# Optimization experiments

Measured on AMD Instinct MI355X. Metric: run time of the kernel, lower is better.

## Reference

```python
import jax, jax.numpy as jnp
import numpy as np
from jax import lax

B, S, D, N_ORDER, K = 8, 4096, 256, 2, 3
G = N_ORDER + 1  # groups in HyenaProjection
EPS_FILT = 1e-8


def setup_inputs() -> dict:
    key = jax.random.key(0)
    ks = jax.random.split(key, 8)
    sc = 0.02
    # positions: per-row arange with trailing -1 padding (one contiguous read per row)
    vl = jnp.where(jnp.arange(B) % 2 == 0, S, (3 * S) // 4)
    pos = jnp.where(jnp.arange(S, dtype=jnp.int32)[None, :] < vl[:, None],
                    jnp.arange(S, dtype=jnp.int32)[None, :], -1)
    return {
        "embeddings": jax.random.normal(ks[0], (B, S, D), jnp.float32),
        "positions": pos,
        "W_proj": jax.random.normal(ks[1], (D, G * D), jnp.float32) * sc,
        "conv_w": jax.random.normal(ks[2], (G * D, D, K), jnp.float32) * sc,
        "conv_b": jnp.zeros((G * D,), jnp.float32),
        "W1": jax.random.normal(ks[3], (D, D), jnp.float32) * sc,
        "b1": jnp.zeros((D,), jnp.float32),
        "ln_g": jnp.ones((D,), jnp.float32),
        "ln_b": jnp.zeros((D,), jnp.float32),
        "W2": jax.random.normal(ks[4], (D, N_ORDER * D), jnp.float32) * sc,
        "b2": jnp.zeros((N_ORDER * D,), jnp.float32),
        "ff_scale": jnp.ones((1, 1, N_ORDER * D), jnp.float32),
        "W_out": jax.random.normal(ks[5], (D, D), jnp.float32) * sc,
        "b_out": jnp.zeros((D,), jnp.float32),
    }


def adjust_positions(pos):
    pf = jnp.where(pos == -1, jnp.inf, pos.astype(jnp.float32))
    minp = pf.min(axis=-1, keepdims=True)
    adj = pos.astype(jnp.float32) - minp
    return jnp.where(pos == -1, -1.0, adj)


def rope_rotate(x, adj_pos):
    # compute_theta_vector + compute_rotation_angles + apply_dimensionwise_rotation
    d2 = x.shape[-1] // 2
    theta = 1.0 / (10000.0 ** (jnp.arange(d2, dtype=jnp.float32) / d2))
    ang = adj_pos[..., None] * theta  # (b, s, d/2)
    cos, sin = jnp.cos(ang), jnp.sin(ang)
    x1, x2 = x[..., 0::2], x[..., 1::2]
    r1 = x1 * cos - x2 * sin
    r2 = x1 * sin + x2 * cos
    return jnp.stack([r1, r2], axis=-1).reshape(x.shape)


def feed_forward(x, W1, b1, ln_g, ln_b, W2, b2, ff_scale):
    h = x @ W1 + b1
    mu = h.mean(-1, keepdims=True)
    var = ((h - mu) ** 2).mean(-1, keepdims=True)
    h = (h - mu) / jnp.sqrt(var + 1e-5) * ln_g + ln_b
    h = jax.nn.gelu(h, approximate=False)
    return (h @ W2 + b2) * ff_scale


def fft_long_conv(x, f, mask):
    # x, f: (b, d, s); 2L zero-padded circular conv == linear conv; torch norm='forward' pair => /n net
    L = x.shape[-1]
    n = 2 * L
    y = jnp.fft.irfft(jnp.fft.rfft(x, n=n) * jnp.fft.rfft(f, n=n), n=n)[..., :L] / n
    return y * mask[:, None, :]


def reference(embeddings, positions, W_proj, conv_w, conv_b, W1, b1, ln_g, ln_b, W2, b2, ff_scale, W_out, b_out):
    mask = (positions != -1).astype(embeddings.dtype)  # (b, s)

    # HyenaProjection: linear -> grouped short conv -> mask -> split into G streams
    z = jnp.einsum('bsd,de->bes', embeddings, W_proj)  # (b, G*d, s)
    z = lax.conv_general_dilated(z, conv_w, (1,), [(K // 2, K // 2)],
                                 dimension_numbers=('NCH', 'OIH', 'NCH'),
                                 feature_group_count=G)
    z = (z + conv_b[None, :, None]) * mask[:, None, :]
    zs = jnp.split(z, G, axis=1)  # G tensors of (b, d, s)

    # HyenaFilter: RoPE -> FFN -> reshape (b, n, d, s) -> L1 normalize over d
    t = rope_rotate(embeddings, adjust_positions(positions))
    h_hat = feed_forward(t, W1, b1, ln_g, ln_b, W2, b2, ff_scale)  # (b, s, n*d)
    h_hat = h_hat.reshape(h_hat.shape[0], h_hat.shape[1], N_ORDER, D).transpose(0, 2, 3, 1)
    h_hat = h_hat / (jnp.sum(jnp.abs(h_hat), axis=2, keepdims=True) + EPS_FILT)

    # Hyena recurrence with FFT long convolutions
    v = zs[-1]
    for i in range(N_ORDER):
        v = zs[i] * fft_long_conv(v, h_hat[:, i], mask)

    out = jnp.einsum('bds,de->bse', v, W_out) + b_out
    return out * mask[..., None]  # reassemble leaves padded positions zero
```

## Files before the change

### kernel.cpp

```cpp
#include <hip/hip_runtime.h>
#include <cstdint>

#define S_LEN 4096
#define D_DIM 256

#define OFF_MINP 0
#define OFF_WPT  16
#define OFF_WTH  (OFF_WPT + 768*256)
#define OFF_WTL  (OFF_WTH + 294912)
#define OFF_C    (OFF_WTL + 294912)
#define OFF_HH   (OFF_C + 8*768*4096)
#define OFF_V    (OFF_HH + 8*2*256*4096)
#define OFF_U    (OFF_V + 8*256*4096)


typedef __attribute__((ext_vector_type(8))) short short8;
typedef __attribute__((ext_vector_type(4))) float f32x4;

__device__ __forceinline__ unsigned int f2bf(float x) {
    union { float f; unsigned int u; } v; v.f = x;
    unsigned int r = v.u + 0x7fffu + ((v.u >> 16) & 1u);
    return r >> 16;
}
__device__ __forceinline__ float bf2f(unsigned int h) {
    union { unsigned int u; float f; } v; v.u = h << 16; return v.f;
}

__global__ __launch_bounds__(256) void k_minpos(const int* __restrict__ pos, float* __restrict__ minp)
{
    const int b = blockIdx.x;
    const int tid = threadIdx.x;
    int mn = 0x7fffffff;
    const int* p = pos + (size_t)b * S_LEN;
    for (int s = tid; s < S_LEN; s += 256) {
        const int v = p[s];
        if (v != -1) mn = min(mn, v);
    }
    __shared__ int red[256];
    red[tid] = mn;
    __syncthreads();
    for (int st = 128; st > 0; st >>= 1) {
        if (tid < st) red[tid] = min(red[tid], red[tid + st]);
        __syncthreads();
    }
    if (tid == 0) minp[b] = (float)red[0];
}

__global__ __launch_bounds__(256) void k_wpt(const float* __restrict__ Wp, float* __restrict__ WpT)
{
    __shared__ float t[32][33];
    const int e0 = blockIdx.x * 32;
    const int d0 = blockIdx.y * 32;
    const int lx = threadIdx.x & 31, ly = threadIdx.x >> 5;
#pragma unroll
    for (int q = 0; q < 4; ++q)
        t[ly + 8*q][lx] = Wp[(size_t)(d0 + ly + 8*q) * 768 + e0 + lx];
    __syncthreads();
#pragma unroll
    for (int q = 0; q < 4; ++q)
        WpT[(size_t)(e0 + ly + 8*q) * 256 + d0 + lx] = t[lx][ly + 8*q];
}

__global__ __launch_bounds__(256) void k_tsplit(const float* __restrict__ W, const int K, const int N,
                                                unsigned short* __restrict__ oh, unsigned short* __restrict__ ol)
{
    __shared__ float t[32][33];
    const int n0 = blockIdx.x * 32;
    const int k0 = blockIdx.y * 32;
    const int lx = threadIdx.x & 31, ly = threadIdx.x >> 5;
#pragma unroll
    for (int q = 0; q < 4; ++q)
        t[ly + 8*q][lx] = W[(size_t)(k0 + ly + 8*q) * N + n0 + lx];
    __syncthreads();
#pragma unroll
    for (int q = 0; q < 4; ++q) {
        const float v = t[lx][ly + 8*q];
        const unsigned int h = f2bf(v);
        oh[(size_t)(n0 + ly + 8*q) * K + k0 + lx] = (unsigned short)h;
        ol[(size_t)(n0 + ly + 8*q) * K + k0 + lx] = (unsigned short)f2bf(v - bf2f(h));
    }
}

__global__ __launch_bounds__(256) void k_weff(const float* __restrict__ WpT, const float* __restrict__ cw,
                                              unsigned short* __restrict__ wth, unsigned short* __restrict__ wtl)
{
    const int o = blockIdx.x;
    const int d = threadIdx.x;
    const int g = o >> 8;
    __shared__ float cwrow[768];
    for (int i = threadIdx.x; i < 768; i += 256) cwrow[i] = cw[(size_t)o * 768 + i];
    __syncthreads();
    float a0 = 0.f, a1 = 0.f, a2 = 0.f;
    const float* wb = WpT + (size_t)(g * 256) * 256 + d;
#pragma unroll 4
    for (int i = 0; i < 256; ++i) {
        const float wv = wb[(size_t)i * 256];
        a0 += wv * cwrow[i*3+0];
        a1 += wv * cwrow[i*3+1];
        a2 += wv * cwrow[i*3+2];
    }
    const float av[3] = {a0, a1, a2};
#pragma unroll
    for (int t = 0; t < 3; ++t) {
        const unsigned int hb = f2bf(av[t]);
        const unsigned int lb = f2bf(av[t] - bf2f(hb));
        wth[(size_t)o * 768 + t * 256 + d] = (unsigned short)hb;
        wtl[(size_t)o * 768 + t * 256 + d] = (unsigned short)lb;
    }
}

#define CG_LDA 40
__global__ __launch_bounds__(256, 3) void k_convgemm(
    const float* __restrict__ emb, const int* __restrict__ pos,
    const unsigned short* __restrict__ wth, const unsigned short* __restrict__ wtl,
    const float* __restrict__ convb, float* __restrict__ c)
{
    const int b  = blockIdx.z;
    const int o0 = blockIdx.y * 128;
    const int s0 = blockIdx.x * 128;
    const int tid  = threadIdx.x;
    const int wave = tid >> 6, lane = tid & 63;
    const int m16  = lane & 15, quad = lane >> 4;

    __shared__ __align__(16) unsigned short As[130 * CG_LDA];
    __shared__ __align__(16) unsigned short Bh[128 * CG_LDA];
    __shared__ __align__(16) unsigned short Bl[128 * CG_LDA];

    const int rA = tid >> 1;
    const int cA = (tid & 1) * 16;
    const int srowA = s0 + rA - 1;
    const bool vA = (srowA >= 0 && srowA < S_LEN);
    const float* embA = emb + ((size_t)b * S_LEN + (vA ? srowA : 0)) * D_DIM + cA;
    const int rT = 128 + (tid >> 3);
    const int cT = (tid & 7) * 4;
    const int srowT = s0 + rT - 1;
    const bool vT = (tid < 16) && (srowT >= 0 && srowT < S_LEN);
    const float* embT = emb + ((size_t)b * S_LEN + ((tid < 16 && vT) ? srowT : 0)) * D_DIM + cT;

    const int rB0 = tid >> 2,        gB0 = (tid & 3) * 8;
    const int rB1 = 64 + (tid >> 2), gB1 = gB0;

    float4 apf[4]; float4 apfT;
    uint4 bph0, bpl0, bph1, bpl1;

#pragma unroll
    for (int q = 0; q < 4; ++q) apf[q] = vA ? *(const float4*)(embA + q * 4) : make_float4(0.f,0.f,0.f,0.f);
    apfT = vT ? *(const float4*)(embT) : make_float4(0.f,0.f,0.f,0.f);
    {
        const size_t gi0 = (size_t)(o0 + rB0) * 768 + gB0;
        const size_t gi1 = (size_t)(o0 + rB1) * 768 + gB1;
        bph0 = *(const uint4*)(wth + gi0); bpl0 = *(const uint4*)(wtl + gi0);
        bph1 = *(const uint4*)(wth + gi1); bpl1 = *(const uint4*)(wtl + gi1);
    }

    f32x4 acc[2][8];
#pragma unroll
    for (int mt = 0; mt < 2; ++mt)
#pragma unroll
        for (int nt = 0; nt < 8; ++nt)
#pragma unroll
            for (int e = 0; e < 4; ++e) acc[mt][nt][e] = 0.f;

    for (int c8 = 0; c8 < 8; ++c8) {
        for (int t = 0; t < 3; ++t) {
            __syncthreads();
            if (t == 0) {
#pragma unroll
                for (int q = 0; q < 4; ++q) {
                    const float4 v = apf[q];
                    uint2 hp;
                    hp.x = f2bf(v.x) | (f2bf(v.y) << 16);
                    hp.y = f2bf(v.z) | (f2bf(v.w) << 16);
                    *(uint2*)&As[rA * CG_LDA + cA + q * 4] = hp;
                }
                if (tid < 16) {
                    const float4 v = apfT;
                    uint2 hp;
                    hp.x = f2bf(v.x) | (f2bf(v.y) << 16);
                    hp.y = f2bf(v.z) | (f2bf(v.w) << 16);
                    *(uint2*)&As[rT * CG_LDA + cT] = hp;
                }
                if (c8 < 7) {
                    const int base = (c8 + 1) * 32;
#pragma unroll
                    for (int q = 0; q < 4; ++q) apf[q] = vA ? *(const float4*)(embA + base + q * 4) : make_float4(0.f,0.f,0.f,0.f);
                    apfT = vT ? *(const float4*)(embT + base) : make_float4(0.f,0.f,0.f,0.f);
                }
            }
            *(uint4*)&Bh[rB0 * CG_LDA + gB0] = bph0;
            *(uint4*)&Bl[rB0 * CG_LDA + gB0] = bpl0;
            *(uint4*)&Bh[rB1 * CG_LDA + gB1] = bph1;
            *(uint4*)&Bl[rB1 * CG_LDA + gB1] = bpl1;
            if (!(c8 == 7 && t == 2)) {
                const int t2  = (t == 2) ? 0 : (t + 1);
                const int c82 = c8 + (t == 2);
                const int kbase = t2 * 256 + c82 * 32;
                const size_t gi0 = (size_t)(o0 + rB0) * 768 + kbase + gB0;
                const size_t gi1 = (size_t)(o0 + rB1) * 768 + kbase + gB1;
                bph0 = *(const uint4*)(wth + gi0); bpl0 = *(const uint4*)(wtl + gi0);
                bph1 = *(const uint4*)(wth + gi1); bpl1 = *(const uint4*)(wtl + gi1);
            }
            __syncthreads();
            short8 ah[2];
#pragma unroll
            for (int mt = 0; mt < 2; ++mt) {
                const int ar = (wave * 32 + mt * 16 + m16 + t) * CG_LDA + quad * 8;
                ah[mt] = *(const short8*)&As[ar];
            }
#pragma unroll
            for (int nt = 0; nt < 8; ++nt) {
                const int br = (nt * 16 + m16) * CG_LDA + quad * 8;
                const short8 bh = *(const short8*)&Bh[br];
                const short8 bl = *(const short8*)&Bl[br];
#pragma unroll
                for (int mt = 0; mt < 2; ++mt) {
                    acc[mt][nt] = __builtin_amdgcn_mfma_f32_16x16x32_bf16(ah[mt], bh, acc[mt][nt], 0, 0, 0);
                    acc[mt][nt] = __builtin_amdgcn_mfma_f32_16x16x32_bf16(ah[mt], bl, acc[mt][nt], 0, 0, 0);
                }
            }
        }
    }
    __syncthreads();

    float msk[2][4];
#pragma unroll
    for (int mt = 0; mt < 2; ++mt) {
        const int s = s0 + wave * 32 + mt * 16 + quad * 4;
        const int4 p4 = *(const int4*)(pos + (size_t)b * S_LEN + s);
        msk[mt][0] = (p4.x != -1) ? 1.f : 0.f;
        msk[mt][1] = (p4.y != -1) ? 1.f : 0.f;
        msk[mt][2] = (p4.z != -1) ? 1.f : 0.f;
        msk[mt][3] = (p4.w != -1) ? 1.f : 0.f;
    }
#pragma unroll
    for (int nt = 0; nt < 8; ++nt) {
        const int o = o0 + nt * 16 + m16;
        const float cb = convb[o];
#pragma unroll
        for (int mt = 0; mt < 2; ++mt) {
            const int s = s0 + wave * 32 + mt * 16 + quad * 4;
            float4 r;
            r.x = (acc[mt][nt][0] + cb) * msk[mt][0];
            r.y = (acc[mt][nt][1] + cb) * msk[mt][1];
            r.z = (acc[mt][nt][2] + cb) * msk[mt][2];
            r.w = (acc[mt][nt][3] + cb) * msk[mt][3];
            *(float4*)(c + ((size_t)(b * 768 + o)) * S_LEN + s) = r;
        }
    }
}

#define FF_LDA 264
#define FF_LDB 136
__global__ __launch_bounds__(256, 2) void k_ff(
    const float* __restrict__ emb, const int* __restrict__ pos, const float* __restrict__ minp,
    const unsigned short* __restrict__ w1th, const unsigned short* __restrict__ w1tl,
    const float* __restrict__ b1,
    const float* __restrict__ lng, const float* __restrict__ lnb,
    const unsigned short* __restrict__ w2th, const unsigned short* __restrict__ w2tl,
    const float* __restrict__ b2, const float* __restrict__ ffs, float* __restrict__ hh)
{
    const int b   = blockIdx.y;
    const int s0  = blockIdx.x * 64;
    const int tid = threadIdx.x;
    const int wave = tid >> 6, lane = tid & 63;
    const int m16  = lane & 15, quad = lane >> 4;

    __shared__ __align__(16) unsigned short Th[64 * FF_LDA];
    __shared__ __align__(16) unsigned short Bsh[16 * FF_LDB];
    __shared__ __align__(16) unsigned short Bsl[16 * FF_LDB];
    __shared__ float th_s[128];

    if (tid < 128) th_s[tid] = expf(-(float)tid * 0.07195578415606394f);
    __syncthreads();

    {
        const int r    = tid >> 2;
        const int col0 = (tid & 3) * 64;
        const int s    = s0 + r;
        const int p    = pos[(size_t)b * S_LEN + s];
        const float adj = (p == -1) ? -1.f : ((float)p - minp[b]);
        const float* ep = emb + ((size_t)b * S_LEN + s) * D_DIM;
#pragma unroll
        for (int p8 = 0; p8 < 8; ++p8) {
            const int cbase = col0 + p8 * 8;
            const float4 va = *(const float4*)(ep + cbase);
            const float4 vb4 = *(const float4*)(ep + cbase + 4);
            const float x[8] = {va.x, va.y, va.z, va.w, vb4.x, vb4.y, vb4.z, vb4.w};
            unsigned int uh[4];
#pragma unroll
            for (int jj = 0; jj < 4; ++jj) {
                const int j = (cbase >> 1) + jj;
                const float theta = th_s[j];
                float sn, cs;
                sincosf(adj * theta, &sn, &cs);
                const float x1 = x[2*jj], x2 = x[2*jj+1];
                const float r1 = x1 * cs - x2 * sn;
                const float r2 = x1 * sn + x2 * cs;
                uh[jj] = f2bf(r1) | (f2bf(r2) << 16);
            }
            uint4 wh;
            wh.x = uh[0]; wh.y = uh[1]; wh.z = uh[2]; wh.w = uh[3];
            *(uint4*)&Th[r * FF_LDA + cbase] = wh;
        }
    }
    __syncthreads();

    const int rowA  = wave * 16 + m16;
    const int strow = tid >> 4;
    const int stks  = (tid & 15) * 8;

    f32x4 acc1[16];
#pragma unroll
    for (int nt = 0; nt < 16; ++nt)
#pragma unroll
        for (int e = 0; e < 4; ++e) acc1[nt][e] = 0.f;

    uint4 pfh, pfl;
    {
        const size_t gi = (size_t)strow * 256 + stks;
        pfh = *(const uint4*)(w1th + gi);
        pfl = *(const uint4*)(w1tl + gi);
    }
    for (int kh = 0; kh < 2; ++kh) {
        short8 a1h[4];
#pragma unroll
        for (int c4 = 0; c4 < 4; ++c4) {
            const int ar = rowA * FF_LDA + kh * 128 + c4 * 32 + quad * 8;
            a1h[c4] = *(const short8*)&Th[ar];
        }
#pragma unroll
        for (int nt = 0; nt < 16; ++nt) {
            __syncthreads();
            *(uint4*)&Bsh[strow * FF_LDB + stks] = pfh;
            *(uint4*)&Bsl[strow * FF_LDB + stks] = pfl;
            if (!(kh == 1 && nt == 15)) {
                const int nt2 = (nt + 1) & 15;
                const int kh2 = kh + (nt == 15);
                const size_t gi = (size_t)(nt2 * 16 + strow) * 256 + kh2 * 128 + stks;
                pfh = *(const uint4*)(w1th + gi);
                pfl = *(const uint4*)(w1tl + gi);
            }
            __syncthreads();
#pragma unroll
            for (int c4 = 0; c4 < 4; ++c4) {
                const int br = m16 * FF_LDB + c4 * 32 + quad * 8;
                const short8 bh = *(const short8*)&Bsh[br];
                const short8 bl = *(const short8*)&Bsl[br];
                acc1[nt] = __builtin_amdgcn_mfma_f32_16x16x32_bf16(a1h[c4], bh, acc1[nt], 0, 0, 0);
                acc1[nt] = __builtin_amdgcn_mfma_f32_16x16x32_bf16(a1h[c4], bl, acc1[nt], 0, 0, 0);
            }
        }
    }

    float sume[4] = {0.f, 0.f, 0.f, 0.f}, sumq[4] = {0.f, 0.f, 0.f, 0.f};
#pragma unroll
    for (int nt = 0; nt < 16; ++nt) {
        const float bb = b1[nt * 16 + m16];
#pragma unroll
        for (int e = 0; e < 4; ++e) {
            const float v = acc1[nt][e] + bb;
            acc1[nt][e] = v;
            sume[e] += v;
            sumq[e] += v * v;
        }
    }
#pragma unroll
    for (int e = 0; e < 4; ++e) {
#pragma unroll
        for (int off = 1; off < 16; off <<= 1) {
            sume[e] += __shfl_xor(sume[e], off, 64);
            sumq[e] += __shfl_xor(sumq[e], off, 64);
        }
    }
    float mu[4], rs[4];
#pragma unroll
    for (int e = 0; e < 4; ++e) {
        mu[e] = sume[e] * (1.f / 256.f);
        const float var = sumq[e] * (1.f / 256.f) - mu[e] * mu[e];
        rs[e] = rsqrtf(var + 1e-5f);
    }

    {
        const size_t gi = (size_t)strow * 256 + stks;
        pfh = *(const uint4*)(w2th + gi);
        pfl = *(const uint4*)(w2tl + gi);
    }

    __syncthreads();
#pragma unroll
    for (int nt = 0; nt < 16; ++nt) {
        const int col = nt * 16 + m16;
        const float g  = lng[col];
        const float be = lnb[col];
#pragma unroll
        for (int e = 0; e < 4; ++e) {
            const float h  = (acc1[nt][e] - mu[e]) * rs[e] * g + be;
            const float hg = 0.5f * h * (1.f + erff(h * 0.7071067811865475f));
            const int li = (wave * 16 + quad * 4 + e) * FF_LDA + col;
            Th[li] = (unsigned short)f2bf(hg);
        }
    }
    __syncthreads();

    f32x4 acc2[32];
#pragma unroll
    for (int nt = 0; nt < 32; ++nt)
#pragma unroll
        for (int e = 0; e < 4; ++e) acc2[nt][e] = 0.f;

    for (int kh = 0; kh < 2; ++kh) {
        short8 a2h[4];
#pragma unroll
        for (int c4 = 0; c4 < 4; ++c4) {
            const int ar = rowA * FF_LDA + kh * 128 + c4 * 32 + quad * 8;
            a2h[c4] = *(const short8*)&Th[ar];
        }
#pragma unroll
        for (int nt = 0; nt < 32; ++nt) {
            __syncthreads();
            *(uint4*)&Bsh[strow * FF_LDB + stks] = pfh;
            *(uint4*)&Bsl[strow * FF_LDB + stks] = pfl;
            if (!(kh == 1 && nt == 31)) {
                const int nt2 = (nt + 1) & 31;
                const int kh2 = kh + (nt == 31);
                const size_t gi = (size_t)(nt2 * 16 + strow) * 256 + kh2 * 128 + stks;
                pfh = *(const uint4*)(w2th + gi);
                pfl = *(const uint4*)(w2tl + gi);
            }
            __syncthreads();
#pragma unroll
            for (int c4 = 0; c4 < 4; ++c4) {
                const int br = m16 * FF_LDB + c4 * 32 + quad * 8;
                const short8 bh = *(const short8*)&Bsh[br];
                const short8 bl = *(const short8*)&Bsl[br];
                acc2[nt] = __builtin_amdgcn_mfma_f32_16x16x32_bf16(a2h[c4], bh, acc2[nt], 0, 0, 0);
                acc2[nt] = __builtin_amdgcn_mfma_f32_16x16x32_bf16(a2h[c4], bl, acc2[nt], 0, 0, 0);
            }
        }
    }

    float sm[2][4] = {{0.f,0.f,0.f,0.f},{0.f,0.f,0.f,0.f}};
#pragma unroll
    for (int nt = 0; nt < 32; ++nt) {
        const int col = nt * 16 + m16;
        const float bb = b2[col];
        const float fs = ffs[col];
#pragma unroll
        for (int e = 0; e < 4; ++e) {
            const float v = (acc2[nt][e] + bb) * fs;
            acc2[nt][e] = v;
            sm[nt >> 4][e] += fabsf(v);
        }
    }
#pragma unroll
    for (int i = 0; i < 2; ++i)
#pragma unroll
        for (int e = 0; e < 4; ++e) {
#pragma unroll
            for (int off = 1; off < 16; off <<= 1)
                sm[i][e] += __shfl_xor(sm[i][e], off, 64);
        }
#pragma unroll
    for (int nt = 0; nt < 32; ++nt) {
        const int i = nt >> 4;
        const int d = (nt & 15) * 16 + m16;
        float4 o4;
        o4.x = acc2[nt][0] / (sm[i][0] + 1e-8f);
        o4.y = acc2[nt][1] / (sm[i][1] + 1e-8f);
        o4.z = acc2[nt][2] / (sm[i][2] + 1e-8f);
        o4.w = acc2[nt][3] / (sm[i][3] + 1e-8f);
        *(float4*)(hh + ((size_t)((b * 2 + i) * 256 + d)) * S_LEN + s0 + wave * 16 + quad * 4) = o4;
    }
}

#define XS_PAD   960
#define XS_ELEMS 5056
#define FRX_WORDS 4160
__device__ __forceinline__ int xsw(int blk) { return blk ^ ((blk >> 3) & 7); }

__global__ __launch_bounds__(64) void k_conv_mfma(
    const float* __restrict__ xbuf, const int xC, const int xoff,
    const float* __restrict__ hh, const int iord,
    const float* __restrict__ cbuf, float* __restrict__ outb)
{
    const int d = blockIdx.x;
    const int b = blockIdx.y;
    const int lane = threadIdx.x;
    const float* xp = xbuf + ((size_t)(b * xC + xoff + d)) * S_LEN;
    const float* fp = hh   + ((size_t)((b * 2 + iord) * 256 + d)) * S_LEN;
    const float* zp = cbuf + ((size_t)(b * 768 + iord * 256 + d)) * S_LEN;
    float* op = outb + ((size_t)(b * 256 + d)) * S_LEN;

    __shared__ unsigned short xs[XS_ELEMS];
    __shared__ unsigned int   frx[FRX_WORDS];

    {
        for (int blk = lane; blk < 120; blk += 64) {
            int4 z; z.x = 0; z.y = 0; z.z = 0; z.w = 0;
            *(int4*)(xs + xsw(blk) * 8) = z;
        }
#pragma unroll
        for (int it = 0; it < 8; ++it) {
            const int idx = it * 64 + lane;
            const int j = idx * 8;
            const float4 v0 = *(const float4*)(xp + j);
            const float4 v1 = *(const float4*)(xp + j + 4);
            int4 w;
            w.x = (int)(f2bf(v0.x) | (f2bf(v0.y) << 16));
            w.y = (int)(f2bf(v0.z) | (f2bf(v0.w) << 16));
            w.z = (int)(f2bf(v1.x) | (f2bf(v1.y) << 16));
            w.w = (int)(f2bf(v1.z) | (f2bf(v1.w) << 16));
            *(int4*)(xs + xsw(120 + idx) * 8) = w;
        }
    }
    {
        frx[4096 + lane] = 0u;
        if (lane == 0) frx[4095] = f2bf(fp[0]);
#pragma unroll
        for (int it = 0; it < 16; ++it) {
            const int j = (it * 64 + lane) * 4;
            const float4 v = *(const float4*)(fp + j);
            const float f4 = (j + 4 < S_LEN) ? fp[j + 4] : 0.f;
            frx[4094 - j] = f2bf(v.y) | (f2bf(v.x) << 16);
            frx[4093 - j] = f2bf(v.z) | (f2bf(v.y) << 16);
            frx[4092 - j] = f2bf(v.w) | (f2bf(v.z) << 16);
            if (j < 4092) frx[4091 - j] = f2bf(f4) | (f2bf(v.w) << 16);
        }
    }
    __syncthreads();

    const int m    = lane & 15;
    const int quad = lane >> 4;

    f32x4 acc[4][4];
#pragma unroll
    for (int mt = 0; mt < 4; ++mt)
#pragma unroll
        for (int pt = 0; pt < 4; ++pt)
#pragma unroll
            for (int e = 0; e < 4; ++e) acc[mt][pt][e] = 0.f;

    const int eA_base = 4095 - m + quad * 8;
    const int oB_base = XS_PAD + 64 * m + quad * 8;

    for (int r = 0; r < 64; ++r) {
        const int ea_r = eA_base - 64 * r;
        short8 afr[4][2];
#pragma unroll
        for (int mt = 0; mt < 4; ++mt)
#pragma unroll
            for (int kc = 0; kc < 2; ++kc) {
                const int e = ea_r - 16 * mt + 32 * kc;
                union { unsigned int u[4]; short8 s; } cvt;
                cvt.u[0] = frx[e];
                cvt.u[1] = frx[e + 2];
                cvt.u[2] = frx[e + 4];
                cvt.u[3] = frx[e + 6];
                afr[mt][kc] = cvt.s;
            }
        const int ptmin = r >> 4;
        const int ob_r = oB_base - 64 * r;
#pragma unroll
        for (int pt = 0; pt < 4; ++pt) {
            if (pt >= ptmin) {
                const int o0 = ob_r + 1024 * pt;
                const short8 bfr0 = *(const short8*)(xs + xsw(o0 >> 3) * 8);
                const short8 bfr1 = *(const short8*)(xs + xsw((o0 + 32) >> 3) * 8);
#pragma unroll
                for (int mt = 0; mt < 4; ++mt) {
                    acc[mt][pt] = __builtin_amdgcn_mfma_f32_16x16x32_bf16(afr[mt][0], bfr0, acc[mt][pt], 0, 0, 0);
                    acc[mt][pt] = __builtin_amdgcn_mfma_f32_16x16x32_bf16(afr[mt][1], bfr1, acc[mt][pt], 0, 0, 0);
                }
            }
        }
    }

    const float inv = 1.f / 8192.f;
#pragma unroll
    for (int mt = 0; mt < 4; ++mt)
#pragma unroll
        for (int pt = 0; pt < 4; ++pt) {
            const int p  = 16 * pt + m;
            const int s0 = 64 * p + 16 * mt + quad * 4;
            const float4 z4 = *(const float4*)(zp + s0);
            float4 o4;
            o4.x = z4.x * acc[mt][pt][0] * inv;
            o4.y = z4.y * acc[mt][pt][1] * inv;
            o4.z = z4.z * acc[mt][pt][2] * inv;
            o4.w = z4.w * acc[mt][pt][3] * inv;
            *(float4*)(op + s0) = o4;
        }
}

__global__ __launch_bounds__(256) void k_out(
    const float* __restrict__ v, const float* __restrict__ Wo,
    const float* __restrict__ bo, const int* __restrict__ pos,
    float* __restrict__ out)
{
    const int b   = blockIdx.y;
    const int s0  = blockIdx.x * 32;
    const int tid = threadIdx.x;
    __shared__ float vs[256 * 36];
    {
        const float4* src = (const float4*)(v + ((size_t)(b*256 + tid)) * S_LEN + s0);
#pragma unroll
        for (int q = 0; q < 8; ++q) {
            *(float4*)&vs[tid*36 + q*4] = src[q];
        }
    }
    __syncthreads();
    float acc[32];
#pragma unroll
    for (int r = 0; r < 32; ++r) acc[r] = 0.f;
    for (int dd = 0; dd < 256; ++dd) {
        const float w = Wo[(size_t)dd * 256 + tid];
        const float* vr = &vs[dd * 36];
#pragma unroll
        for (int q = 0; q < 8; ++q) {
            const float4 x4 = *(const float4*)&vr[q*4];
            acc[q*4+0] += x4.x * w;
            acc[q*4+1] += x4.y * w;
            acc[q*4+2] += x4.z * w;
            acc[q*4+3] += x4.w * w;
        }
    }
    const float bb = bo[tid];
#pragma unroll
    for (int r = 0; r < 32; ++r) {
        const int s = s0 + r;
        const float m = (pos[(size_t)b * S_LEN + s] != -1) ? 1.f : 0.f;
        out[((size_t)b * S_LEN + s) * 256 + tid] = (acc[r] + bb) * m;
    }
}

extern "C" void kernel_launch(void* const* d_in, const int* in_sizes, int n_in,
                              void* d_out, int out_size, void* d_ws, size_t ws_size,
                              hipStream_t stream) {
    const float* emb = (const float*)d_in[0];
    const int*   pos = (const int*)  d_in[1];
    const float* Wp  = (const float*)d_in[2];
    const float* cw  = (const float*)d_in[3];
    const float* cb  = (const float*)d_in[4];
    const float* W1  = (const float*)d_in[5];
    const float* b1  = (const float*)d_in[6];
    const float* lg  = (const float*)d_in[7];
    const float* lb  = (const float*)d_in[8];
    const float* W2  = (const float*)d_in[9];
    const float* b2  = (const float*)d_in[10];
    const float* ffs = (const float*)d_in[11];
    const float* Wo  = (const float*)d_in[12];
    const float* bo  = (const float*)d_in[13];

    float* ws   = (float*)d_ws;
    float* minp = ws + OFF_MINP;
    float* wpt  = ws + OFF_WPT;
    unsigned short* wth = (unsigned short*)(ws + OFF_WTH);
    unsigned short* wtl = (unsigned short*)(ws + OFF_WTL);
    float* c    = ws + OFF_C;
    float* hh   = ws + OFF_HH;
    float* vb   = ws + OFF_V;
    float* ub   = ws + OFF_U;

    unsigned short* w1th = (unsigned short*)vb;
    unsigned short* w1tl = w1th + 256 * 256;
    unsigned short* w2th = w1tl + 256 * 256;
    unsigned short* w2tl = w2th + 512 * 256;

    k_minpos<<<dim3(8), dim3(256), 0, stream>>>(pos, minp);
    k_wpt<<<dim3(24, 8), dim3(256), 0, stream>>>(Wp, wpt);
    k_weff<<<dim3(768), dim3(256), 0, stream>>>(wpt, cw, wth, wtl);
    k_tsplit<<<dim3(8, 8), dim3(256), 0, stream>>>(W1, 256, 256, w1th, w1tl);
    k_tsplit<<<dim3(16, 8), dim3(256), 0, stream>>>(W2, 256, 512, w2th, w2tl);
    k_convgemm<<<dim3(32, 6, 8), dim3(256), 0, stream>>>(emb, pos, wth, wtl, cb, c);
    k_ff<<<dim3(64, 8), dim3(256), 0, stream>>>(emb, pos, minp, w1th, w1tl, b1, lg, lb, w2th, w2tl, b2, ffs, hh);
    k_conv_mfma<<<dim3(256, 8), dim3(64), 0, stream>>>(c, 768, 512, hh, 0, c, vb);
    k_conv_mfma<<<dim3(256, 8), dim3(64), 0, stream>>>(vb, 256, 0, hh, 1, c, ub);
    k_out<<<dim3(128, 8), dim3(256), 0, stream>>>(ub, Wo, bo, pos, (float*)d_out);
}
```

Measured before the change: 534.9 us.

## Split causal conv MFMA reduction loop across two waves per block

The long-convolution MFMA kernel now launches two waves per block, and each wave handles alternating row tiles of the Toeplitz product. Shared-memory staging of the input and filter is divided between the 128 threads. At the end, wave 1 writes its partial accumulators into the reused filter LDS buffer and wave 0 sums them, then applies the gating and writes the output. The aim is more latency hiding and shorter per-block critical paths, at the cost of an extra LDS reduction and barriers.

```diff
diff --git a/kernel.cpp b/kernel.cpp
--- a/kernel.cpp
+++ b/kernel.cpp
@@ -478,30 +478,32 @@
 #define FRX_WORDS 4160
 __device__ __forceinline__ int xsw(int blk) { return blk ^ ((blk >> 3) & 7); }
 
-__global__ __launch_bounds__(64) void k_conv_mfma(
+__global__ __launch_bounds__(128) void k_conv_mfma(
     const float* __restrict__ xbuf, const int xC, const int xoff,
     const float* __restrict__ hh, const int iord,
     const float* __restrict__ cbuf, float* __restrict__ outb)
 {
     const int d = blockIdx.x;
     const int b = blockIdx.y;
-    const int lane = threadIdx.x;
+    const int tid  = threadIdx.x;
+    const int lane = tid & 63;
+    const int wid  = tid >> 6;
     const float* xp = xbuf + ((size_t)(b * xC + xoff + d)) * S_LEN;
     const float* fp = hh   + ((size_t)((b * 2 + iord) * 256 + d)) * S_LEN;
     const float* zp = cbuf + ((size_t)(b * 768 + iord * 256 + d)) * S_LEN;
     float* op = outb + ((size_t)(b * 256 + d)) * S_LEN;
 
-    __shared__ unsigned short xs[XS_ELEMS];
-    __shared__ unsigned int   frx[FRX_WORDS];
+    __shared__ __align__(16) unsigned short xs[XS_ELEMS];
+    __shared__ __align__(16) unsigned int   frx[FRX_WORDS];
 
     {
-        for (int blk = lane; blk < 120; blk += 64) {
+        for (int blk = tid; blk < 120; blk += 128) {
             int4 z; z.x = 0; z.y = 0; z.z = 0; z.w = 0;
             *(int4*)(xs + xsw(blk) * 8) = z;
         }
 #pragma unroll
-        for (int it = 0; it < 8; ++it) {
-            const int idx = it * 64 + lane;
+        for (int it = 0; it < 4; ++it) {
+            const int idx = it * 128 + tid;
             const int j = idx * 8;
             const float4 v0 = *(const float4*)(xp + j);
             const float4 v1 = *(const float4*)(xp + j + 4);
@@ -514,11 +516,11 @@
         }
     }
     {
-        frx[4096 + lane] = 0u;
-        if (lane == 0) frx[4095] = f2bf(fp[0]);
-#pragma unroll
-        for (int it = 0; it < 16; ++it) {
-            const int j = (it * 64 + lane) * 4;
+        if (tid < 64) frx[4096 + tid] = 0u;
+        if (tid == 0) frx[4095] = f2bf(fp[0]);
+#pragma unroll
+        for (int it = 0; it < 8; ++it) {
+            const int j = (it * 128 + tid) * 4;
             const float4 v = *(const float4*)(fp + j);
             const float f4 = (j + 4 < S_LEN) ? fp[j + 4] : 0.f;
             frx[4094 - j] = f2bf(v.y) | (f2bf(v.x) << 16);
@@ -543,7 +545,8 @@
     const int eA_base = 4095 - m + quad * 8;
     const int oB_base = XS_PAD + 64 * m + quad * 8;
 
-    for (int r = 0; r < 64; ++r) {
+    for (int i = 0; i < 32; ++i) {
+        const int r = 2 * i + wid;
         const int ea_r = eA_base - 64 * r;
         short8 afr[4][2];
 #pragma unroll
@@ -575,21 +578,34 @@
         }
     }
 
-    const float inv = 1.f / 8192.f;
-#pragma unroll
-    for (int mt = 0; mt < 4; ++mt)
-#pragma unroll
-        for (int pt = 0; pt < 4; ++pt) {
-            const int p  = 16 * pt + m;
-            const int s0 = 64 * p + 16 * mt + quad * 4;
-            const float4 z4 = *(const float4*)(zp + s0);
-            float4 o4;
-            o4.x = z4.x * acc[mt][pt][0] * inv;
-            o4.y = z4.y * acc[mt][pt][1] * inv;
-            o4.z = z4.z * acc[mt][pt][2] * inv;
-            o4.w = z4.w * acc[mt][pt][3] * inv;
-            *(float4*)(op + s0) = o4;
-        }
+    __syncthreads();
+    float* red = (float*)frx;
+    if (wid == 1) {
+#pragma unroll
+        for (int mt = 0; mt < 4; ++mt)
+#pragma unroll
+            for (int pt = 0; pt < 4; ++pt)
+                *(f32x4*)&red[((mt * 4 + pt) * 64 + lane) * 4] = acc[mt][pt];
+    }
+    __syncthreads();
+    if (wid == 0) {
+        const float inv = 1.f / 8192.f;
+#pragma unroll
+        for (int mt = 0; mt < 4; ++mt)
+#pragma unroll
+            for (int pt = 0; pt < 4; ++pt) {
+                const f32x4 po = *(const f32x4*)&red[((mt * 4 + pt) * 64 + lane) * 4];
+                const int p  = 16 * pt + m;
+                const int s0 = 64 * p + 16 * mt + quad * 4;
+                const float4 z4 = *(const float4*)(zp + s0);
+                float4 o4;
+                o4.x = z4.x * (acc[mt][pt][0] + po[0]) * inv;
+                o4.y = z4.y * (acc[mt][pt][1] + po[1]) * inv;
+                o4.z = z4.z * (acc[mt][pt][2] + po[2]) * inv;
+                o4.w = z4.w * (acc[mt][pt][3] + po[3]) * inv;
+                *(float4*)(op + s0) = o4;
+            }
+    }
 }
 
 __global__ __launch_bounds__(256) void k_out(
@@ -673,7 +689,7 @@
     k_tsplit<<<dim3(16, 8), dim3(256), 0, stream>>>(W2, 256, 512, w2th, w2tl);
     k_convgemm<<<dim3(32, 6, 8), dim3(256), 0, stream>>>(emb, pos, wth, wtl, cb, c);
     k_ff<<<dim3(64, 8), dim3(256), 0, stream>>>(emb, pos, minp, w1th, w1tl, b1, lg, lb, w2th, w2tl, b2, ffs, hh);
-    k_conv_mfma<<<dim3(256, 8), dim3(64), 0, stream>>>(c, 768, 512, hh, 0, c, vb);
-    k_conv_mfma<<<dim3(256, 8), dim3(64), 0, stream>>>(vb, 256, 0, hh, 1, c, ub);
+    k_conv_mfma<<<dim3(256, 8), dim3(128), 0, stream>>>(c, 768, 512, hh, 0, c, vb);
+    k_conv_mfma<<<dim3(256, 8), dim3(128), 0, stream>>>(vb, 256, 0, hh, 1, c, ub);
     k_out<<<dim3(128, 8), dim3(256), 0, stream>>>(ub, Wo, bo, pos, (float*)d_out);
 }
```

New measurement: 511.9 us. -4.3%, faster.
